# Kernel optimization log

Measured on AMD Instinct MI355X. Metric: run time of the kernel, lower is better.

## Reference

```python
import jax, jax.numpy as jnp
import numpy as np

B, S, F_IN, E = 8, 1024, 256, 512
INNER = 2 * E            # mLSTM proj_factor = 2.0
NH = 4                   # mLSTM num_heads
DH = INNER // NH
KS = 4                   # causal conv1d kernel size
QKV_BS = 4               # qkv_proj_blocksize
NB = INNER // QKV_BS     # number of block-diagonal qkv blocks


def setup_inputs() -> dict:
    key = jax.random.key(0)
    ks = jax.random.split(key, 16)
    g = lambda k, shape, scale: jax.random.normal(k, shape, jnp.float32) * scale
    return {
        "x": g(ks[0], (B, S, F_IN), 1.0),
        "W_in": g(ks[1], (E, F_IN), F_IN ** -0.5),
        "b_in": jnp.zeros((E,), jnp.float32),
        "ln1_w": jnp.ones((E,), jnp.float32),
        "W_up": g(ks[2], (2 * INNER, E), E ** -0.5),
        "conv_w": g(ks[3], (INNER, 1, KS), KS ** -0.5),
        "conv_b": jnp.zeros((INNER,), jnp.float32),
        "Wq": g(ks[4], (NB, QKV_BS, QKV_BS), QKV_BS ** -0.5),
        "Wk": g(ks[5], (NB, QKV_BS, QKV_BS), QKV_BS ** -0.5),
        "Wv": g(ks[6], (NB, QKV_BS, QKV_BS), QKV_BS ** -0.5),
        "W_ig": g(ks[7], (NH, 3 * INNER), (3 * INNER) ** -0.5),
        "b_ig": jnp.zeros((NH,), jnp.float32),
        "W_fg": g(ks[8], (NH, 3 * INNER), (3 * INNER) ** -0.5),
        "b_fg": jnp.linspace(3.0, 6.0, NH, dtype=jnp.float32),  # xlstm fgate bias init
        "mhln_w": jnp.ones((INNER,), jnp.float32),
        "skip": jnp.ones((INNER,), jnp.float32),
        "W_down": g(ks[9], (E, INNER), INNER ** -0.5),
        "ln_post_w": jnp.ones((E,), jnp.float32),
    }


def _ln(h, w, eps=1e-5):
    m = h.mean(-1, keepdims=True)
    v = jnp.mean((h - m) ** 2, axis=-1, keepdims=True)
    return (h - m) * jax.lax.rsqrt(v + eps) * w


def _causal_conv(x, w, b):
    # x: (B,S,C) -> depthwise causal conv, kernel KS, left-pad KS-1
    y = jax.lax.conv_general_dilated(
        x.transpose(0, 2, 1), w, (1,), [(KS - 1, 0)],
        dimension_numbers=("NCH", "OIH", "NCH"), feature_group_count=INNER)
    return y.transpose(0, 2, 1) + b


def _headwise(x, W):
    # block-diagonal linear (LinearHeadwiseExpand, bias=False)
    b, s, _ = x.shape
    xh = x.reshape(b, s, NB, QKV_BS)
    return jnp.einsum("bsni,noi->bsno", xh, W).reshape(b, s, -1)


def reference(x, W_in, b_in, ln1_w, W_up, conv_w, conv_b, Wq, Wk, Wv,
              W_ig, b_ig, W_fg, b_fg, mhln_w, skip, W_down, ln_post_w):
    # input proj (+ dropout = identity in eval)
    xp = x @ W_in.T + b_in                                  # (B,S,E)
    res = xp
    h = _ln(xp, ln1_w)                                      # pre-LN of mLSTM block
    up = h @ W_up.T                                         # (B,S,2*INNER)
    x_m, z = up[..., :INNER], up[..., INNER:]
    xc = jax.nn.silu(_causal_conv(x_m, conv_w, conv_b))     # (B,S,INNER)
    q = _headwise(xc, Wq)
    k = _headwise(xc, Wk)
    v = _headwise(x_m, Wv)
    gate_in = jnp.concatenate([q, k, v], axis=-1)           # (B,S,3*INNER)
    ig = (gate_in @ W_ig.T + b_ig).transpose(0, 2, 1)       # (B,NH,S)
    fg = (gate_in @ W_fg.T + b_fg).transpose(0, 2, 1)       # (B,NH,S)
    to_h = lambda t: t.reshape(B, S, NH, DH).transpose(0, 2, 1, 3)
    qh, kh, vh = to_h(q), to_h(k), to_h(v)                  # (B,NH,S,DH)
    # --- parallel_stabilized_simple mLSTM backend ---
    logf = jax.nn.log_sigmoid(fg)                           # (B,NH,S)
    a = jnp.concatenate([jnp.zeros_like(logf[..., :1]), jnp.cumsum(logf, -1)], -1)
    M = a[..., :, None] - a[..., None, :]                   # (B,NH,S+1,S+1)
    mask = jnp.tril(jnp.ones((S + 1, S + 1), bool))
    logD = jnp.where(mask, M, -jnp.inf)[..., 1:, 1:] + ig[..., None, :]
    maxD = logD.max(-1, keepdims=True)                      # (B,NH,S,1)
    D = jnp.exp(logD - maxD)
    C = jnp.einsum("bnsd,bntd->bnst", qh, kh * (DH ** -0.5)) * D
    n = jnp.maximum(jnp.abs(C.sum(-1, keepdims=True)), jnp.exp(-maxD))
    hh = jnp.einsum("bnst,bntd->bnsd", C / (n + 1e-6), vh)  # (B,NH,S,DH)
    # multi-head layernorm (GroupNorm per head, weight only, bias-free)
    hn = hh.transpose(0, 2, 1, 3)                           # (B,S,NH,DH)
    mu = hn.mean(-1, keepdims=True)
    var = jnp.mean((hn - mu) ** 2, axis=-1, keepdims=True)
    hn = (hn - mu) * jax.lax.rsqrt(var + 1e-5) * mhln_w.reshape(NH, DH)
    hn = hn.reshape(B, S, INNER)
    h_state = (hn + skip * xc) * jax.nn.silu(z)             # learnable skip + output gate
    y = h_state @ W_down.T                                  # (B,S,E)
    out = res + y                                           # residual
    return _ln(out, ln_post_w)                              # post_blocks_norm
```

## Files before the change

### kernel.cpp

```cpp
#include <hip/hip_runtime.h>

#define S_LEN 1024
#define B_SZ 8
#define F_IN_D 256
#define E_DIM 512
#define INNER_D 1024
#define NH_D 4
#define DH_D 256
#define NROW (B_SZ * S_LEN)

typedef _Float16 half8 __attribute__((ext_vector_type(8)));
typedef _Float16 half4_t __attribute__((ext_vector_type(4)));
typedef float v4f __attribute__((ext_vector_type(4)));

__global__ __launch_bounds__(256) void cast4_kernel(
    const float* __restrict__ s0, const float* __restrict__ s1,
    const float* __restrict__ s2, const float* __restrict__ s3,
    _Float16* __restrict__ d0, _Float16* __restrict__ d1,
    _Float16* __restrict__ d2, _Float16* __restrict__ d3,
    int n0, int n1, int n2, int n3)
{
  int i = (blockIdx.x * 256 + threadIdx.x) * 4;
  const float* s; _Float16* d; int off;
  if (i < n0)                { s = s0; d = d0; off = i; }
  else if (i < n0 + n1)      { s = s1; d = d1; off = i - n0; }
  else if (i < n0 + n1 + n2) { s = s2; d = d2; off = i - n0 - n1; }
  else if (i < n0 + n1 + n2 + n3) { s = s3; d = d3; off = i - n0 - n1 - n2; }
  else return;
  float4 v = *(const float4*)(s + off);
  half4_t o = {(_Float16)v.x, (_Float16)v.y, (_Float16)v.z, (_Float16)v.w};
  *(half4_t*)(d + off) = o;
}

#define GBM 128
#define GBN 128
#define GBK 64
#define LDKG (GBK + 8)

__global__ __launch_bounds__(256) void gemm_h16(
    const _Float16* __restrict__ A, const _Float16* __restrict__ B,
    const float* __restrict__ bias, float* __restrict__ C,
    int M, int N, int K)
{
  __shared__ __align__(16) _Float16 As[GBM][LDKG];
  __shared__ __align__(16) _Float16 Bs[GBN][LDKG];
  const int tid = threadIdx.x;
  const int lane = tid & 63, w = tid >> 6;
  const int wr = w >> 1, wc = w & 1;
  const int quad = lane >> 4, l16 = lane & 15;
  const int bm = blockIdx.y * GBM, bn = blockIdx.x * GBN;
  const int srow = tid >> 1;
  const int scol = (tid & 1) * 32;

  v4f acc[4][4];
#pragma unroll
  for (int i = 0; i < 4; ++i)
#pragma unroll
    for (int j = 0; j < 4; ++j) acc[i][j] = (v4f){0.f, 0.f, 0.f, 0.f};

  const _Float16* Ap = A + (size_t)(bm + srow) * K + scol;
  const _Float16* Bp = B + (size_t)(bn + srow) * K + scol;
  half8 ap[4], bp[4];
#pragma unroll
  for (int j = 0; j < 4; ++j) {
    ap[j] = *(const half8*)(Ap + j * 8);
    bp[j] = *(const half8*)(Bp + j * 8);
  }

  for (int k0 = 0; k0 < K; k0 += GBK) {
    __syncthreads();
#pragma unroll
    for (int j = 0; j < 4; ++j) {
      *(half8*)(&As[srow][scol + j * 8]) = ap[j];
      *(half8*)(&Bs[srow][scol + j * 8]) = bp[j];
    }
    __syncthreads();
    if (k0 + GBK < K) {
      const int kn = k0 + GBK;
#pragma unroll
      for (int j = 0; j < 4; ++j) {
        ap[j] = *(const half8*)(Ap + kn + j * 8);
        bp[j] = *(const half8*)(Bp + kn + j * 8);
      }
    }
#pragma unroll
    for (int kc = 0; kc < 2; ++kc) {
      half8 af[4], bf[4];
#pragma unroll
      for (int i = 0; i < 4; ++i)
        af[i] = *(const half8*)(&As[wr * 64 + i * 16 + l16][kc * 32 + quad * 8]);
#pragma unroll
      for (int j = 0; j < 4; ++j)
        bf[j] = *(const half8*)(&Bs[wc * 64 + j * 16 + l16][kc * 32 + quad * 8]);
#pragma unroll
      for (int i = 0; i < 4; ++i)
#pragma unroll
        for (int j = 0; j < 4; ++j)
          acc[i][j] = __builtin_amdgcn_mfma_f32_16x16x32_f16(af[i], bf[j], acc[i][j], 0, 0, 0);
    }
  }

#pragma unroll
  for (int j = 0; j < 4; ++j) {
    const int col = bn + wc * 64 + j * 16 + l16;
    const float bv = bias ? bias[col] : 0.f;
#pragma unroll
    for (int i = 0; i < 4; ++i) {
      const int row0 = bm + wr * 64 + i * 16 + quad * 4;
#pragma unroll
      for (int r = 0; r < 4; ++r)
        C[(size_t)(row0 + r) * N + col] = acc[i][j][r] + bv;
    }
  }
}

__global__ __launch_bounds__(256) void gemm_h16_up(
    const _Float16* __restrict__ A, const _Float16* __restrict__ B,
    _Float16* __restrict__ xmh, _Float16* __restrict__ szb,
    int M, int N, int K)
{
  __shared__ __align__(16) _Float16 As[GBM][LDKG];
  __shared__ __align__(16) _Float16 Bs[GBN][LDKG];
  const int tid = threadIdx.x;
  const int lane = tid & 63, w = tid >> 6;
  const int wr = w >> 1, wc = w & 1;
  const int quad = lane >> 4, l16 = lane & 15;
  const int bm = blockIdx.y * GBM, bn = blockIdx.x * GBN;
  const int srow = tid >> 1;
  const int scol = (tid & 1) * 32;

  v4f acc[4][4];
#pragma unroll
  for (int i = 0; i < 4; ++i)
#pragma unroll
    for (int j = 0; j < 4; ++j) acc[i][j] = (v4f){0.f, 0.f, 0.f, 0.f};

  const _Float16* Ap = A + (size_t)(bm + srow) * K + scol;
  const _Float16* Bp = B + (size_t)(bn + srow) * K + scol;
  half8 ap[4], bp[4];
#pragma unroll
  for (int j = 0; j < 4; ++j) {
    ap[j] = *(const half8*)(Ap + j * 8);
    bp[j] = *(const half8*)(Bp + j * 8);
  }

  for (int k0 = 0; k0 < K; k0 += GBK) {
    __syncthreads();
#pragma unroll
    for (int j = 0; j < 4; ++j) {
      *(half8*)(&As[srow][scol + j * 8]) = ap[j];
      *(half8*)(&Bs[srow][scol + j * 8]) = bp[j];
    }
    __syncthreads();
    if (k0 + GBK < K) {
      const int kn = k0 + GBK;
#pragma unroll
      for (int j = 0; j < 4; ++j) {
        ap[j] = *(const half8*)(Ap + kn + j * 8);
        bp[j] = *(const half8*)(Bp + kn + j * 8);
      }
    }
#pragma unroll
    for (int kc = 0; kc < 2; ++kc) {
      half8 af[4], bf[4];
#pragma unroll
      for (int i = 0; i < 4; ++i)
        af[i] = *(const half8*)(&As[wr * 64 + i * 16 + l16][kc * 32 + quad * 8]);
#pragma unroll
      for (int j = 0; j < 4; ++j)
        bf[j] = *(const half8*)(&Bs[wc * 64 + j * 16 + l16][kc * 32 + quad * 8]);
#pragma unroll
      for (int i = 0; i < 4; ++i)
#pragma unroll
        for (int j = 0; j < 4; ++j)
          acc[i][j] = __builtin_amdgcn_mfma_f32_16x16x32_f16(af[i], bf[j], acc[i][j], 0, 0, 0);
    }
  }

  const bool zhalf = (bn >= INNER_D);
#pragma unroll
  for (int j = 0; j < 4; ++j) {
    const int col = bn + wc * 64 + j * 16 + l16;
    const int colm = col & (INNER_D - 1);
#pragma unroll
    for (int i = 0; i < 4; ++i) {
      const int row0 = bm + wr * 64 + i * 16 + quad * 4;
#pragma unroll
      for (int r = 0; r < 4; ++r) {
        float a = acc[i][j][r];
        if (zhalf) {
          float s = a / (1.f + __expf(-a));
          szb[(size_t)(row0 + r) * INNER_D + colm] = (_Float16)s;
        } else {
          xmh[(size_t)(row0 + r) * INNER_D + colm] = (_Float16)a;
        }
      }
    }
  }
}

__device__ __forceinline__ float block_sum4(float v, float* red, int tid) {
#pragma unroll
  for (int off = 32; off; off >>= 1) v += __shfl_xor(v, off);
  if ((tid & 63) == 0) red[tid >> 6] = v;
  __syncthreads();
  float t = red[0] + red[1] + red[2] + red[3];
  __syncthreads();
  return t;
}

__global__ __launch_bounds__(256) void ln_mul_kernel(
    const float* __restrict__ in, const float* __restrict__ w,
    _Float16* __restrict__ out)
{
  __shared__ float red[4];
  const int row = blockIdx.x;
  const int tid = threadIdx.x;
  const float* p = in + (size_t)row * E_DIM;
  float v0 = p[tid], v1 = p[tid + 256];
  float mean = block_sum4(v0 + v1, red, tid) * (1.f / E_DIM);
  float d0 = v0 - mean, d1 = v1 - mean;
  float var = block_sum4(d0 * d0 + d1 * d1, red, tid) * (1.f / E_DIM);
  float rstd = rsqrtf(var + 1e-5f);
  out[(size_t)row * E_DIM + tid] = (_Float16)(d0 * rstd * w[tid]);
  out[(size_t)row * E_DIM + tid + 256] = (_Float16)(d1 * rstd * w[tid + 256]);
}

__global__ __launch_bounds__(256) void final_ln_kernel(
    const float* __restrict__ res, const float* __restrict__ y,
    const float* __restrict__ w, float* __restrict__ out)
{
  __shared__ float red[4];
  const int row = blockIdx.x;
  const int tid = threadIdx.x;
  const size_t base = (size_t)row * E_DIM;
  float v0 = res[base + tid] + y[base + tid];
  float v1 = res[base + tid + 256] + y[base + tid + 256];
  float mean = block_sum4(v0 + v1, red, tid) * (1.f / E_DIM);
  float d0 = v0 - mean, d1 = v1 - mean;
  float var = block_sum4(d0 * d0 + d1 * d1, red, tid) * (1.f / E_DIM);
  float rstd = rsqrtf(var + 1e-5f);
  out[base + tid] = d0 * rstd * w[tid];
  out[base + tid + 256] = d1 * rstd * w[tid + 256];
}

__global__ __launch_bounds__(256) void chg_kernel(
    const _Float16* __restrict__ xm, const float* __restrict__ cw,
    const float* __restrict__ cb,
    const float* __restrict__ Wq, const float* __restrict__ Wk,
    const float* __restrict__ Wv,
    const float* __restrict__ Wig, const float* __restrict__ big,
    const float* __restrict__ Wfg, const float* __restrict__ bfg,
    _Float16* __restrict__ xch, _Float16* __restrict__ qh,
    _Float16* __restrict__ khb, _Float16* __restrict__ vhb,
    float* __restrict__ ig, float* __restrict__ fg)
{
  __shared__ float red[4][32];
  const int tid = threadIdx.x;
  const int lane = tid & 63, wid = tid >> 6;
  const int row0 = blockIdx.x * 4;
  const int sl0 = row0 & (S_LEN - 1);
  const int c = tid * 4;

  float t[7][4];
#pragma unroll
  for (int j = 0; j < 7; ++j) {
    const int off = j - 3;
    if (sl0 + off < 0) {
      t[j][0] = t[j][1] = t[j][2] = t[j][3] = 0.f;
    } else {
      half4_t hv = *(const half4_t*)(xm + (size_t)(row0 + off) * INNER_D + c);
      t[j][0] = (float)hv.x; t[j][1] = (float)hv.y;
      t[j][2] = (float)hv.z; t[j][3] = (float)hv.w;
    }
  }
  float wct[4][4];
#pragma unroll
  for (int j = 0; j < 4; ++j) {
    float4 wc4 = *(const float4*)(cw + (c + j) * 4);
    wct[j][0] = wc4.x; wct[j][1] = wc4.y; wct[j][2] = wc4.z; wct[j][3] = wc4.w;
  }
  float4 cb4 = *(const float4*)(cb + c);
  const float cbs[4] = {cb4.x, cb4.y, cb4.z, cb4.w};
  float wqm[16], wkm[16], wvm[16];
#pragma unroll
  for (int i = 0; i < 4; ++i) {
    float4 a = *(const float4*)(Wq + tid * 16 + i * 4);
    float4 bq = *(const float4*)(Wk + tid * 16 + i * 4);
    float4 cq = *(const float4*)(Wv + tid * 16 + i * 4);
    wqm[i * 4] = a.x; wqm[i * 4 + 1] = a.y; wqm[i * 4 + 2] = a.z; wqm[i * 4 + 3] = a.w;
    wkm[i * 4] = bq.x; wkm[i * 4 + 1] = bq.y; wkm[i * 4 + 2] = bq.z; wkm[i * 4 + 3] = bq.w;
    wvm[i * 4] = cq.x; wvm[i * 4 + 1] = cq.y; wvm[i * 4 + 2] = cq.z; wvm[i * 4 + 3] = cq.w;
  }

  float q4[4][4], k4[4][4], v4m[4][4];
#pragma unroll
  for (int r = 0; r < 4; ++r) {
    float xc4[4];
#pragma unroll
    for (int j = 0; j < 4; ++j) {
      float a = cbs[j] + wct[j][0] * t[r][j] + wct[j][1] * t[r + 1][j]
                       + wct[j][2] * t[r + 2][j] + wct[j][3] * t[r + 3][j];
      xc4[j] = a / (1.f + __expf(-a));
    }
#pragma unroll
    for (int i = 0; i < 4; ++i) {
      q4[r][i] = wqm[i * 4] * xc4[0] + wqm[i * 4 + 1] * xc4[1]
               + wqm[i * 4 + 2] * xc4[2] + wqm[i * 4 + 3] * xc4[3];
      k4[r][i] = wkm[i * 4] * xc4[0] + wkm[i * 4 + 1] * xc4[1]
               + wkm[i * 4 + 2] * xc4[2] + wkm[i * 4 + 3] * xc4[3];
      v4m[r][i] = wvm[i * 4] * t[r + 3][0] + wvm[i * 4 + 1] * t[r + 3][1]
                + wvm[i * 4 + 2] * t[r + 3][2] + wvm[i * 4 + 3] * t[r + 3][3];
    }
    const size_t base = (size_t)(row0 + r) * INNER_D + c;
    half4_t xo = {(_Float16)xc4[0], (_Float16)xc4[1], (_Float16)xc4[2], (_Float16)xc4[3]};
    half4_t qo = {(_Float16)q4[r][0], (_Float16)q4[r][1], (_Float16)q4[r][2], (_Float16)q4[r][3]};
    half4_t ko = {(_Float16)k4[r][0], (_Float16)k4[r][1], (_Float16)k4[r][2], (_Float16)k4[r][3]};
    half4_t vo = {(_Float16)v4m[r][0], (_Float16)v4m[r][1], (_Float16)v4m[r][2], (_Float16)v4m[r][3]};
    *(half4_t*)(xch + base) = xo;
    *(half4_t*)(qh + base) = qo;
    *(half4_t*)(khb + base) = ko;
    *(half4_t*)(vhb + base) = vo;
  }

  float vals[32];
#pragma unroll
  for (int g = 0; g < 8; ++g) {
    const float* wb = (g < 4 ? Wig : Wfg) + (g & 3) * 3072 + c;
    float4 w1 = *(const float4*)(wb);
    float4 w2 = *(const float4*)(wb + 1024);
    float4 w3 = *(const float4*)(wb + 2048);
#pragma unroll
    for (int r = 0; r < 4; ++r) {
      vals[g * 4 + r] =
          q4[r][0] * w1.x + q4[r][1] * w1.y + q4[r][2] * w1.z + q4[r][3] * w1.w
        + k4[r][0] * w2.x + k4[r][1] * w2.y + k4[r][2] * w2.z + k4[r][3] * w2.w
        + v4m[r][0] * w3.x + v4m[r][1] * w3.y + v4m[r][2] * w3.z + v4m[r][3] * w3.w;
    }
  }
#pragma unroll
  for (int i = 0; i < 32; ++i) {
    float x = vals[i];
#pragma unroll
    for (int off = 32; off; off >>= 1) x += __shfl_xor(x, off);
    vals[i] = x;
  }
  if (lane == 0) {
#pragma unroll
    for (int i = 0; i < 32; ++i) red[wid][i] = vals[i];
  }
  __syncthreads();
  if (tid < 32) {
    float sm = red[0][tid] + red[1][tid] + red[2][tid] + red[3][tid];
    const int g = tid >> 2, r = tid & 3;
    const int h = g & 3;
    const int b = row0 >> 10;
    const size_t oidx = (size_t)(b * NH_D + h) * S_LEN + sl0 + r;
    if (g < 4) ig[oidx] = sm + big[h];
    else       fg[oidx] = sm + bfg[h];
  }
}

__device__ __forceinline__ float logsigf(float x) {
  return fminf(x, 0.f) - log1pf(__expf(-fabsf(x)));
}

__global__ __launch_bounds__(256) void scan_kernel(
    const float* __restrict__ ig, const float* __restrict__ fg,
    float* __restrict__ m_, float* __restrict__ rmax_, float* __restrict__ maxd_,
    float* __restrict__ em_)
{
  __shared__ float sc[256];
  const int bh = blockIdx.x;
  const int tid = threadIdx.x;
  const size_t base = (size_t)bh * S_LEN + tid * 4;
  float4 f4 = *(const float4*)(fg + base);
  float4 i4 = *(const float4*)(ig + base);
  float l0 = logsigf(f4.x), l1 = logsigf(f4.y), l2 = logsigf(f4.z), l3 = logsigf(f4.w);
  float p0 = l0, p1 = p0 + l1, p2 = p1 + l2, p3 = p2 + l3;
  sc[tid] = p3;
  __syncthreads();
  for (int off = 1; off < 256; off <<= 1) {
    float o = (tid >= off) ? sc[tid - off] : 0.f;
    __syncthreads();
    sc[tid] += o;
    __syncthreads();
  }
  float aoff = (tid == 0) ? 0.f : sc[tid - 1];
  __syncthreads();
  float a0 = aoff + p0, a1 = aoff + p1, a2 = aoff + p2, a3 = aoff + p3;
  float m0 = i4.x - a0, m1 = i4.y - a1, m2 = i4.z - a2, m3 = i4.w - a3;
  float x0 = m0, x1 = fmaxf(x0, m1), x2 = fmaxf(x1, m2), x3 = fmaxf(x2, m3);
  sc[tid] = x3;
  __syncthreads();
  for (int off = 1; off < 256; off <<= 1) {
    float o = (tid >= off) ? sc[tid - off] : -1e30f;
    __syncthreads();
    sc[tid] = fmaxf(sc[tid], o);
    __syncthreads();
  }
  float moff = (tid == 0) ? -1e30f : sc[tid - 1];
  float tmax = sc[tid | 15];
  float r0 = fmaxf(moff, x0), r1 = fmaxf(moff, x1), r2 = fmaxf(moff, x2), r3 = fmaxf(moff, x3);
  const float scale = 0.0625f;
  float4 mo = {m0, m1, m2, m3};
  float4 ro = {r0, r1, r2, r3};
  float4 dd = {a0 + r0, a1 + r1, a2 + r2, a3 + r3};
  float4 eo = {scale * __expf(m0 - tmax), scale * __expf(m1 - tmax),
               scale * __expf(m2 - tmax), scale * __expf(m3 - tmax)};
  *(float4*)(m_ + base) = mo;
  *(float4*)(rmax_ + base) = ro;
  *(float4*)(maxd_ + base) = dd;
  *(float4*)(em_ + base) = eo;
}

__global__ __launch_bounds__(256) void vtrans_kernel(
    const _Float16* __restrict__ vb, _Float16* __restrict__ vt)
{
  __shared__ _Float16 tile[64][68];
  const int b = blockIdx.z, dt = blockIdx.x, st = blockIdx.y;
  const int c4 = (threadIdx.x & 15) * 4, rr = threadIdx.x >> 4;
  const int s0 = st * 64, d0 = dt * 64;
#pragma unroll
  for (int i = 0; i < 4; ++i) {
    int r = rr + i * 16;
    half4_t v = *(const half4_t*)(vb + ((size_t)(b * S_LEN + s0 + r)) * INNER_D + d0 + c4);
    tile[r][c4 + 0] = v.x; tile[r][c4 + 1] = v.y;
    tile[r][c4 + 2] = v.z; tile[r][c4 + 3] = v.w;
  }
  __syncthreads();
#pragma unroll
  for (int i = 0; i < 4; ++i) {
    int dd = rr + i * 16;
    half4_t o = {tile[c4 + 0][dd], tile[c4 + 1][dd], tile[c4 + 2][dd], tile[c4 + 3][dd]};
    *(half4_t*)(vt + ((size_t)(b * INNER_D + d0 + dd)) * S_LEN + s0 + c4) = o;
  }
}

#define KP 264
#define VP 72
#define PP 72

__global__ __launch_bounds__(256, 2) void attn_blk_kernel(
    const _Float16* __restrict__ qh, const _Float16* __restrict__ khb,
    const _Float16* __restrict__ vt,
    const float* __restrict__ m_, const float* __restrict__ em,
    const float* __restrict__ rmax_, const float* __restrict__ maxd_,
    const float* __restrict__ mhln_w, const float* __restrict__ skip,
    const _Float16* __restrict__ xch, const _Float16* __restrict__ szb,
    _Float16* __restrict__ hstate)
{
  __shared__ __align__(16) _Float16 Ks[64][KP];
  __shared__ __align__(16) _Float16 Vs[256][VP];
  __shared__ __align__(16) _Float16 Pl[64][PP];
  __shared__ float cred[2][64];
  const int tid = threadIdx.x;
  const int lane = tid & 63, wid = tid >> 6;
  const int quad = lane >> 4, l16 = lane & 15;
  const int wr = wid >> 1;
  const int ws = wid & 1;
  const int bh = blockIdx.x & 31;
  int pp = blockIdx.x >> 5;
  if (pp >= 8) pp = 23 - pp;
  const int sblk = 15 - pp;
  const int h = bh & 3, b = bh >> 2;
  const float* rmaxp = rmax_ + (size_t)bh * S_LEN;
  const float* emp = em + (size_t)bh * S_LEN;
  const float* mp = m_ + (size_t)bh * S_LEN;
  const float* maxdp = maxd_ + (size_t)bh * S_LEN;
  const float scale = 0.0625f;

  const _Float16* kg = khb + ((size_t)(b * S_LEN)) * INNER_D + h * DH_D;
  const _Float16* vg = vt + ((size_t)(b * INNER_D + h * DH_D)) * S_LEN;
  const int krow_s = tid >> 5;
  const int kcol_s = (tid & 31) * 8;
  const int vrow_s = tid >> 3;
  const int vcol_s = (tid & 7) * 8;

  const int ntile = sblk + 1;
  const int qb0 = sblk * 64;

  half8 kpre[8], vpre[8];
#pragma unroll
  for (int i = 0; i < 8; ++i) {
    kpre[i] = *(const half8*)(kg + (size_t)(i * 8 + krow_s) * INNER_D + kcol_s);
    vpre[i] = *(const half8*)(vg + (size_t)(i * 32 + vrow_s) * S_LEN + vcol_s);
  }

  half8 qf[2][8];
#pragma unroll
  for (int g = 0; g < 2; ++g) {
    const _Float16* qrow =
        qh + ((size_t)(b * S_LEN + qb0 + wr * 32 + g * 16 + l16)) * INNER_D
           + h * DH_D + quad * 8;
#pragma unroll
    for (int c = 0; c < 8; ++c) qf[g][c] = *(const half8*)(qrow + c * 32);
  }

  v4f acc[2][8];
#pragma unroll
  for (int g = 0; g < 2; ++g)
#pragma unroll
    for (int nc = 0; nc < 8; ++nc) acc[g][nc] = (v4f){0.f, 0.f, 0.f, 0.f};
  float rsum[8] = {0.f, 0.f, 0.f, 0.f, 0.f, 0.f, 0.f, 0.f};
  float rmax_row[8];
#pragma unroll
  for (int g = 0; g < 2; ++g)
#pragma unroll
    for (int r = 0; r < 4; ++r)
      rmax_row[g * 4 + r] = rmaxp[qb0 + wr * 32 + g * 16 + quad * 4 + r];

  for (int tt = 0; tt < ntile; ++tt) {
    const int t0 = tt * 64;
    const bool last = (tt + 1 == ntile);
    __syncthreads();
#pragma unroll
    for (int i = 0; i < 8; ++i) {
      *(half8*)(&Ks[i * 8 + krow_s][kcol_s]) = kpre[i];
      *(half8*)(&Vs[i * 32 + vrow_s][vcol_s]) = vpre[i];
    }
    __syncthreads();
    if (!last) {
      const int tn = t0 + 64;
#pragma unroll
      for (int i = 0; i < 8; ++i) {
        kpre[i] = *(const half8*)(kg + (size_t)(tn + i * 8 + krow_s) * INNER_D + kcol_s);
        vpre[i] = *(const half8*)(vg + (size_t)(i * 32 + vrow_s) * S_LEN + tn + vcol_s);
      }
    }
    float rowfac[8];
    if (!last) {
      const float rtile = rmaxp[t0 + 63];
#pragma unroll
      for (int gr = 0; gr < 8; ++gr) rowfac[gr] = __expf(rtile - rmax_row[gr]);
    }
#pragma unroll
    for (int ks = 0; ks < 2; ++ks) {
      v4f sg[2];
      sg[0] = (v4f){0.f, 0.f, 0.f, 0.f};
      sg[1] = (v4f){0.f, 0.f, 0.f, 0.f};
#pragma unroll
      for (int c = 0; c < 8; ++c) {
        half8 kf = *(const half8*)(&Ks[ws * 32 + ks * 16 + l16][c * 32 + quad * 8]);
        sg[0] = __builtin_amdgcn_mfma_f32_16x16x32_f16(qf[0][c], kf, sg[0], 0, 0, 0);
        sg[1] = __builtin_amdgcn_mfma_f32_16x16x32_f16(qf[1][c], kf, sg[1], 0, 0, 0);
      }
      const int t = t0 + ws * 32 + ks * 16 + l16;
      if (last) {
        const float mt = mp[t];
#pragma unroll
        for (int g = 0; g < 2; ++g)
#pragma unroll
          for (int r = 0; r < 4; ++r) {
            const int srow = qb0 + wr * 32 + g * 16 + quad * 4 + r;
            float cc = (t <= srow)
                         ? sg[g][r] * scale * __expf(mt - rmax_row[g * 4 + r]) : 0.f;
            rsum[g * 4 + r] += cc;
            Pl[wr * 32 + g * 16 + quad * 4 + r][ws * 32 + ks * 16 + l16] = (_Float16)cc;
          }
      } else {
        const float emv = emp[t];
#pragma unroll
        for (int g = 0; g < 2; ++g)
#pragma unroll
          for (int r = 0; r < 4; ++r) {
            float cc = sg[g][r] * emv * rowfac[g * 4 + r];
            rsum[g * 4 + r] += cc;
            Pl[wr * 32 + g * 16 + quad * 4 + r][ws * 32 + ks * 16 + l16] = (_Float16)cc;
          }
      }
    }
    __syncthreads();
    half8 pf[2][2];
#pragma unroll
    for (int g = 0; g < 2; ++g) {
      pf[g][0] = *(const half8*)(&Pl[wr * 32 + g * 16 + l16][quad * 8]);
      pf[g][1] = *(const half8*)(&Pl[wr * 32 + g * 16 + l16][32 + quad * 8]);
    }
#pragma unroll
    for (int nc = 0; nc < 8; ++nc) {
      half8 vf0 = *(const half8*)(&Vs[ws * 128 + nc * 16 + l16][quad * 8]);
      half8 vf1 = *(const half8*)(&Vs[ws * 128 + nc * 16 + l16][32 + quad * 8]);
      acc[0][nc] = __builtin_amdgcn_mfma_f32_16x16x32_f16(pf[0][0], vf0, acc[0][nc], 0, 0, 0);
      acc[0][nc] = __builtin_amdgcn_mfma_f32_16x16x32_f16(pf[0][1], vf1, acc[0][nc], 0, 0, 0);
      acc[1][nc] = __builtin_amdgcn_mfma_f32_16x16x32_f16(pf[1][0], vf0, acc[1][nc], 0, 0, 0);
      acc[1][nc] = __builtin_amdgcn_mfma_f32_16x16x32_f16(pf[1][1], vf1, acc[1][nc], 0, 0, 0);
    }
  }

#pragma unroll
  for (int gr = 0; gr < 8; ++gr) {
    float rs = rsum[gr];
    rs += __shfl_xor(rs, 1); rs += __shfl_xor(rs, 2);
    rs += __shfl_xor(rs, 4); rs += __shfl_xor(rs, 8);
    rsum[gr] = rs;
  }
  if (l16 == 0) {
#pragma unroll
    for (int g = 0; g < 2; ++g)
#pragma unroll
      for (int r = 0; r < 4; ++r)
        cred[ws][wr * 32 + g * 16 + quad * 4 + r] = rsum[g * 4 + r];
  }
  __syncthreads();
  float inv[8];
#pragma unroll
  for (int g = 0; g < 2; ++g)
#pragma unroll
    for (int r = 0; r < 4; ++r) {
      const int row = wr * 32 + g * 16 + quad * 4 + r;
      float rs = cred[0][row] + cred[1][row];
      float md = maxdp[qb0 + row];
      float n = fmaxf(fabsf(rs), __expf(-md));
      inv[g * 4 + r] = 1.f / (n + 1e-6f);
    }
#pragma unroll
  for (int g = 0; g < 2; ++g)
#pragma unroll
    for (int nc = 0; nc < 8; ++nc)
#pragma unroll
      for (int r = 0; r < 4; ++r) acc[g][nc][r] *= inv[g * 4 + r];

  __syncthreads();
  float mean[8];
#pragma unroll
  for (int gr = 0; gr < 8; ++gr) {
    const int g = gr >> 2, r = gr & 3;
    float sm = 0.f;
#pragma unroll
    for (int nc = 0; nc < 8; ++nc) sm += acc[g][nc][r];
    sm += __shfl_xor(sm, 1); sm += __shfl_xor(sm, 2);
    sm += __shfl_xor(sm, 4); sm += __shfl_xor(sm, 8);
    if (l16 == 0) cred[ws][wr * 32 + g * 16 + quad * 4 + r] = sm;
  }
  __syncthreads();
#pragma unroll
  for (int gr = 0; gr < 8; ++gr) {
    const int g = gr >> 2, r = gr & 3;
    const int row = wr * 32 + g * 16 + quad * 4 + r;
    mean[gr] = (cred[0][row] + cred[1][row]) * (1.f / DH_D);
  }
  __syncthreads();
  float rstd[8];
#pragma unroll
  for (int gr = 0; gr < 8; ++gr) {
    const int g = gr >> 2, r = gr & 3;
    float sq = 0.f;
#pragma unroll
    for (int nc = 0; nc < 8; ++nc) { float d = acc[g][nc][r] - mean[gr]; sq += d * d; }
    sq += __shfl_xor(sq, 1); sq += __shfl_xor(sq, 2);
    sq += __shfl_xor(sq, 4); sq += __shfl_xor(sq, 8);
    if (l16 == 0) cred[ws][wr * 32 + g * 16 + quad * 4 + r] = sq;
  }
  __syncthreads();
#pragma unroll
  for (int gr = 0; gr < 8; ++gr) {
    const int g = gr >> 2, r = gr & 3;
    const int row = wr * 32 + g * 16 + quad * 4 + r;
    rstd[gr] = rsqrtf((cred[0][row] + cred[1][row]) * (1.f / DH_D) + 1e-5f);
  }

#pragma unroll
  for (int nc = 0; nc < 8; ++nc) {
    const int d = h * DH_D + ws * 128 + nc * 16 + l16;
    const float w = mhln_w[d];
    const float sk = skip[d];
#pragma unroll
    for (int g = 0; g < 2; ++g)
#pragma unroll
      for (int r = 0; r < 4; ++r) {
        const size_t row = (size_t)(b * S_LEN + qb0 + wr * 32 + g * 16 + quad * 4 + r);
        float xcv = (float)xch[row * INNER_D + d];
        float sz = (float)szb[row * INNER_D + d];
        float o = ((acc[g][nc][r] - mean[g * 4 + r]) * rstd[g * 4 + r] * w + sk * xcv) * sz;
        hstate[row * INNER_D + d] = (_Float16)o;
      }
  }
}

extern "C" void kernel_launch(void* const* d_in, const int* in_sizes, int n_in,
                              void* d_out, int out_size, void* d_ws, size_t ws_size,
                              hipStream_t stream)
{
  const float* x      = (const float*)d_in[0];
  const float* W_in   = (const float*)d_in[1];
  const float* b_in   = (const float*)d_in[2];
  const float* ln1_w  = (const float*)d_in[3];
  const float* W_up   = (const float*)d_in[4];
  const float* conv_w = (const float*)d_in[5];
  const float* conv_b = (const float*)d_in[6];
  const float* Wq     = (const float*)d_in[7];
  const float* Wk     = (const float*)d_in[8];
  const float* Wv     = (const float*)d_in[9];
  const float* W_ig   = (const float*)d_in[10];
  const float* b_ig   = (const float*)d_in[11];
  const float* W_fg   = (const float*)d_in[12];
  const float* b_fg   = (const float*)d_in[13];
  const float* mhln_w = (const float*)d_in[14];
  const float* skip   = (const float*)d_in[15];
  const float* W_down = (const float*)d_in[16];
  const float* ln_post_w = (const float*)d_in[17];
  float* out = (float*)d_out;

  float* ws = (float*)d_ws;
  size_t o = 0;
  float* xp     = ws + o; o += (size_t)NROW * E_DIM;
  float* hbuf   = ws + o; o += (size_t)NROW * E_DIM;
  _Float16* h16 = (_Float16*)(ws + o);
  size_t ho = 0;
  _Float16* xh      = h16 + ho; ho += (size_t)NROW * F_IN_D;
  _Float16* WinH    = h16 + ho; ho += (size_t)E_DIM * F_IN_D;
  _Float16* WupH    = h16 + ho; ho += (size_t)2 * INNER_D * E_DIM;
  _Float16* WdownH  = h16 + ho; ho += (size_t)E_DIM * INNER_D;
  _Float16* hh      = h16 + ho; ho += (size_t)NROW * E_DIM;
  _Float16* xmh     = h16 + ho; ho += (size_t)NROW * INNER_D;
  _Float16* szb     = h16 + ho; ho += (size_t)NROW * INNER_D;
  _Float16* xch     = h16 + ho; ho += (size_t)NROW * INNER_D;
  _Float16* qh      = h16 + ho; ho += (size_t)NROW * INNER_D;
  _Float16* khb     = h16 + ho; ho += (size_t)NROW * INNER_D;
  _Float16* vhb     = h16 + ho; ho += (size_t)NROW * INNER_D;
  _Float16* vtb     = h16 + ho; ho += (size_t)NROW * INNER_D;
  _Float16* hstateH = h16 + ho; ho += (size_t)NROW * INNER_D;

  const int GSZ = B_SZ * NH_D * S_LEN;
  float* igb   = hbuf;
  float* fgb   = hbuf + GSZ;
  float* mb    = hbuf + 2 * GSZ;
  float* rmaxb = hbuf + 3 * GSZ;
  float* maxdb = hbuf + 4 * GSZ;
  float* emb   = hbuf + 5 * GSZ;
  float* yb    = hbuf;

  dim3 blk(256);
  const int nx = NROW * F_IN_D, nwi = E_DIM * F_IN_D,
            nwu = 2 * INNER_D * E_DIM, nwd = E_DIM * INNER_D;
  const int ntot = nx + nwi + nwu + nwd;
  cast4_kernel<<<(ntot / 4 + 255) / 256, blk, 0, stream>>>(
      x, W_in, W_up, W_down, xh, WinH, WupH, WdownH, nx, nwi, nwu, nwd);
  gemm_h16<<<dim3(E_DIM / GBN, NROW / GBM), blk, 0, stream>>>(
      xh, WinH, b_in, xp, NROW, E_DIM, F_IN_D);
  ln_mul_kernel<<<NROW, blk, 0, stream>>>(xp, ln1_w, hh);
  gemm_h16_up<<<dim3(2 * INNER_D / GBN, NROW / GBM), blk, 0, stream>>>(
      hh, WupH, xmh, szb, NROW, 2 * INNER_D, E_DIM);
  chg_kernel<<<NROW / 4, blk, 0, stream>>>(
      xmh, conv_w, conv_b, Wq, Wk, Wv, W_ig, b_ig, W_fg, b_fg,
      xch, qh, khb, vhb, igb, fgb);
  scan_kernel<<<B_SZ * NH_D, blk, 0, stream>>>(igb, fgb, mb, rmaxb, maxdb, emb);
  vtrans_kernel<<<dim3(16, 16, 8), blk, 0, stream>>>(vhb, vtb);
  attn_blk_kernel<<<512, blk, 0, stream>>>(
      qh, khb, vtb, mb, emb, rmaxb, maxdb, mhln_w, skip, xch, szb, hstateH);
  gemm_h16<<<dim3(E_DIM / GBN, NROW / GBM), blk, 0, stream>>>(
      hstateH, WdownH, nullptr, yb, NROW, E_DIM, INNER_D);
  final_ln_kernel<<<NROW, blk, 0, stream>>>(xp, yb, ln_post_w, out);
}
```

Measured before the change: 283.9 us.

## Pair complementary query blocks in one 512-thread attention workgroup sharing K/V tiles

Each attention workgroup now holds two 4-wave groups that process complementary causal query blocks (j and 15-j) of the same batch-head. Both groups share each K/V tile staged in LDS, so K/V global loads and LDS staging are amortised over two query blocks. Every block also gets a balanced total of causal work. In exchange, the short-block group sits idle at barriers for the tiles beyond its causal range, the block size doubles with one block per CU, and the grid halves to 256 blocks, which can lower latency hiding.

```diff
diff --git a/kernel.cpp b/kernel.cpp
--- a/kernel.cpp
+++ b/kernel.cpp
@@ -441,7 +441,7 @@
 #define VP 72
 #define PP 72
 
-__global__ __launch_bounds__(256, 2) void attn_blk_kernel(
+__global__ __launch_bounds__(512, 1) void attn_blk_kernel(
     const _Float16* __restrict__ qh, const _Float16* __restrict__ khb,
     const _Float16* __restrict__ vt,
     const float* __restrict__ m_, const float* __restrict__ em,
@@ -452,17 +452,20 @@
 {
   __shared__ __align__(16) _Float16 Ks[64][KP];
   __shared__ __align__(16) _Float16 Vs[256][VP];
-  __shared__ __align__(16) _Float16 Pl[64][PP];
-  __shared__ float cred[2][64];
+  __shared__ __align__(16) _Float16 Pl[2][64][PP];
+  __shared__ float cred[2][2][64];
   const int tid = threadIdx.x;
   const int lane = tid & 63, wid = tid >> 6;
   const int quad = lane >> 4, l16 = lane & 15;
-  const int wr = wid >> 1;
+  const int grp = wid >> 2;
+  const int wr = (wid >> 1) & 1;
   const int ws = wid & 1;
-  const int bh = blockIdx.x & 31;
-  int pp = blockIdx.x >> 5;
-  if (pp >= 8) pp = 23 - pp;
-  const int sblk = 15 - pp;
+  const int bh = blockIdx.x >> 3;
+  const int j = blockIdx.x & 7;
+  const int qblk = grp ? j : (15 - j);
+  const int ntile = qblk + 1;
+  const int Tmax = 16 - j;
+  const int qb0 = qblk * 64;
   const int h = bh & 3, b = bh >> 2;
   const float* rmaxp = rmax_ + (size_t)bh * S_LEN;
   const float* emp = em + (size_t)bh * S_LEN;
@@ -477,14 +480,11 @@
   const int vrow_s = tid >> 3;
   const int vcol_s = (tid & 7) * 8;
 
-  const int ntile = sblk + 1;
-  const int qb0 = sblk * 64;
-
-  half8 kpre[8], vpre[8];
-#pragma unroll
-  for (int i = 0; i < 8; ++i) {
-    kpre[i] = *(const half8*)(kg + (size_t)(i * 8 + krow_s) * INNER_D + kcol_s);
-    vpre[i] = *(const half8*)(vg + (size_t)(i * 32 + vrow_s) * S_LEN + vcol_s);
+  half8 kpre[4], vpre[4];
+#pragma unroll
+  for (int i = 0; i < 4; ++i) {
+    kpre[i] = *(const half8*)(kg + (size_t)(i * 16 + krow_s) * INNER_D + kcol_s);
+    vpre[i] = *(const half8*)(vg + (size_t)(i * 64 + vrow_s) * S_LEN + vcol_s);
   }
 
   half8 qf[2][8];
@@ -510,81 +510,86 @@
     for (int r = 0; r < 4; ++r)
       rmax_row[g * 4 + r] = rmaxp[qb0 + wr * 32 + g * 16 + quad * 4 + r];
 
-  for (int tt = 0; tt < ntile; ++tt) {
+  for (int tt = 0; tt < Tmax; ++tt) {
     const int t0 = tt * 64;
-    const bool last = (tt + 1 == ntile);
-    __syncthreads();
-#pragma unroll
-    for (int i = 0; i < 8; ++i) {
-      *(half8*)(&Ks[i * 8 + krow_s][kcol_s]) = kpre[i];
-      *(half8*)(&Vs[i * 32 + vrow_s][vcol_s]) = vpre[i];
-    }
-    __syncthreads();
-    if (!last) {
+    const bool active = (tt < ntile);
+    const bool diag = (tt == ntile - 1);
+    __syncthreads();
+#pragma unroll
+    for (int i = 0; i < 4; ++i) {
+      *(half8*)(&Ks[i * 16 + krow_s][kcol_s]) = kpre[i];
+      *(half8*)(&Vs[i * 64 + vrow_s][vcol_s]) = vpre[i];
+    }
+    __syncthreads();
+    if (tt + 1 < Tmax) {
       const int tn = t0 + 64;
 #pragma unroll
-      for (int i = 0; i < 8; ++i) {
-        kpre[i] = *(const half8*)(kg + (size_t)(tn + i * 8 + krow_s) * INNER_D + kcol_s);
-        vpre[i] = *(const half8*)(vg + (size_t)(i * 32 + vrow_s) * S_LEN + tn + vcol_s);
-      }
-    }
-    float rowfac[8];
-    if (!last) {
-      const float rtile = rmaxp[t0 + 63];
-#pragma unroll
-      for (int gr = 0; gr < 8; ++gr) rowfac[gr] = __expf(rtile - rmax_row[gr]);
-    }
-#pragma unroll
-    for (int ks = 0; ks < 2; ++ks) {
-      v4f sg[2];
-      sg[0] = (v4f){0.f, 0.f, 0.f, 0.f};
-      sg[1] = (v4f){0.f, 0.f, 0.f, 0.f};
-#pragma unroll
-      for (int c = 0; c < 8; ++c) {
-        half8 kf = *(const half8*)(&Ks[ws * 32 + ks * 16 + l16][c * 32 + quad * 8]);
-        sg[0] = __builtin_amdgcn_mfma_f32_16x16x32_f16(qf[0][c], kf, sg[0], 0, 0, 0);
-        sg[1] = __builtin_amdgcn_mfma_f32_16x16x32_f16(qf[1][c], kf, sg[1], 0, 0, 0);
-      }
-      const int t = t0 + ws * 32 + ks * 16 + l16;
-      if (last) {
-        const float mt = mp[t];
-#pragma unroll
-        for (int g = 0; g < 2; ++g)
-#pragma unroll
-          for (int r = 0; r < 4; ++r) {
-            const int srow = qb0 + wr * 32 + g * 16 + quad * 4 + r;
-            float cc = (t <= srow)
-                         ? sg[g][r] * scale * __expf(mt - rmax_row[g * 4 + r]) : 0.f;
-            rsum[g * 4 + r] += cc;
-            Pl[wr * 32 + g * 16 + quad * 4 + r][ws * 32 + ks * 16 + l16] = (_Float16)cc;
-          }
-      } else {
-        const float emv = emp[t];
-#pragma unroll
-        for (int g = 0; g < 2; ++g)
-#pragma unroll
-          for (int r = 0; r < 4; ++r) {
-            float cc = sg[g][r] * emv * rowfac[g * 4 + r];
-            rsum[g * 4 + r] += cc;
-            Pl[wr * 32 + g * 16 + quad * 4 + r][ws * 32 + ks * 16 + l16] = (_Float16)cc;
-          }
-      }
-    }
-    __syncthreads();
-    half8 pf[2][2];
-#pragma unroll
-    for (int g = 0; g < 2; ++g) {
-      pf[g][0] = *(const half8*)(&Pl[wr * 32 + g * 16 + l16][quad * 8]);
-      pf[g][1] = *(const half8*)(&Pl[wr * 32 + g * 16 + l16][32 + quad * 8]);
-    }
-#pragma unroll
-    for (int nc = 0; nc < 8; ++nc) {
-      half8 vf0 = *(const half8*)(&Vs[ws * 128 + nc * 16 + l16][quad * 8]);
-      half8 vf1 = *(const half8*)(&Vs[ws * 128 + nc * 16 + l16][32 + quad * 8]);
-      acc[0][nc] = __builtin_amdgcn_mfma_f32_16x16x32_f16(pf[0][0], vf0, acc[0][nc], 0, 0, 0);
-      acc[0][nc] = __builtin_amdgcn_mfma_f32_16x16x32_f16(pf[0][1], vf1, acc[0][nc], 0, 0, 0);
-      acc[1][nc] = __builtin_amdgcn_mfma_f32_16x16x32_f16(pf[1][0], vf0, acc[1][nc], 0, 0, 0);
-      acc[1][nc] = __builtin_amdgcn_mfma_f32_16x16x32_f16(pf[1][1], vf1, acc[1][nc], 0, 0, 0);
+      for (int i = 0; i < 4; ++i) {
+        kpre[i] = *(const half8*)(kg + (size_t)(tn + i * 16 + krow_s) * INNER_D + kcol_s);
+        vpre[i] = *(const half8*)(vg + (size_t)(i * 64 + vrow_s) * S_LEN + tn + vcol_s);
+      }
+    }
+    if (active) {
+      float rowfac[8];
+      if (!diag) {
+        const float rtile = rmaxp[t0 + 63];
+#pragma unroll
+        for (int gr = 0; gr < 8; ++gr) rowfac[gr] = __expf(rtile - rmax_row[gr]);
+      }
+#pragma unroll
+      for (int ks = 0; ks < 2; ++ks) {
+        v4f sg[2];
+        sg[0] = (v4f){0.f, 0.f, 0.f, 0.f};
+        sg[1] = (v4f){0.f, 0.f, 0.f, 0.f};
+#pragma unroll
+        for (int c = 0; c < 8; ++c) {
+          half8 kf = *(const half8*)(&Ks[ws * 32 + ks * 16 + l16][c * 32 + quad * 8]);
+          sg[0] = __builtin_amdgcn_mfma_f32_16x16x32_f16(qf[0][c], kf, sg[0], 0, 0, 0);
+          sg[1] = __builtin_amdgcn_mfma_f32_16x16x32_f16(qf[1][c], kf, sg[1], 0, 0, 0);
+        }
+        const int t = t0 + ws * 32 + ks * 16 + l16;
+        if (diag) {
+          const float mt = mp[t];
+#pragma unroll
+          for (int g = 0; g < 2; ++g)
+#pragma unroll
+            for (int r = 0; r < 4; ++r) {
+              const int srow = qb0 + wr * 32 + g * 16 + quad * 4 + r;
+              float cc = (t <= srow)
+                           ? sg[g][r] * scale * __expf(mt - rmax_row[g * 4 + r]) : 0.f;
+              rsum[g * 4 + r] += cc;
+              Pl[grp][wr * 32 + g * 16 + quad * 4 + r][ws * 32 + ks * 16 + l16] = (_Float16)cc;
+            }
+        } else {
+          const float emv = emp[t];
+#pragma unroll
+          for (int g = 0; g < 2; ++g)
+#pragma unroll
+            for (int r = 0; r < 4; ++r) {
+              float cc = sg[g][r] * emv * rowfac[g * 4 + r];
+              rsum[g * 4 + r] += cc;
+              Pl[grp][wr * 32 + g * 16 + quad * 4 + r][ws * 32 + ks * 16 + l16] = (_Float16)cc;
+            }
+        }
+      }
+    }
+    __syncthreads();
+    if (active) {
+      half8 pf[2][2];
+#pragma unroll
+      for (int g = 0; g < 2; ++g) {
+        pf[g][0] = *(const half8*)(&Pl[grp][wr * 32 + g * 16 + l16][quad * 8]);
+        pf[g][1] = *(const half8*)(&Pl[grp][wr * 32 + g * 16 + l16][32 + quad * 8]);
+      }
+#pragma unroll
+      for (int nc = 0; nc < 8; ++nc) {
+        half8 vf0 = *(const half8*)(&Vs[ws * 128 + nc * 16 + l16][quad * 8]);
+        half8 vf1 = *(const half8*)(&Vs[ws * 128 + nc * 16 + l16][32 + quad * 8]);
+        acc[0][nc] = __builtin_amdgcn_mfma_f32_16x16x32_f16(pf[0][0], vf0, acc[0][nc], 0, 0, 0);
+        acc[0][nc] = __builtin_amdgcn_mfma_f32_16x16x32_f16(pf[0][1], vf1, acc[0][nc], 0, 0, 0);
+        acc[1][nc] = __builtin_amdgcn_mfma_f32_16x16x32_f16(pf[1][0], vf0, acc[1][nc], 0, 0, 0);
+        acc[1][nc] = __builtin_amdgcn_mfma_f32_16x16x32_f16(pf[1][1], vf1, acc[1][nc], 0, 0, 0);
+      }
     }
   }
 
@@ -600,7 +605,7 @@
     for (int g = 0; g < 2; ++g)
 #pragma unroll
       for (int r = 0; r < 4; ++r)
-        cred[ws][wr * 32 + g * 16 + quad * 4 + r] = rsum[g * 4 + r];
+        cred[grp][ws][wr * 32 + g * 16 + quad * 4 + r] = rsum[g * 4 + r];
   }
   __syncthreads();
   float inv[8];
@@ -609,7 +614,7 @@
 #pragma unroll
     for (int r = 0; r < 4; ++r) {
       const int row = wr * 32 + g * 16 + quad * 4 + r;
-      float rs = cred[0][row] + cred[1][row];
+      float rs = cred[grp][0][row] + cred[grp][1][row];
       float md = maxdp[qb0 + row];
       float n = fmaxf(fabsf(rs), __expf(-md));
       inv[g * 4 + r] = 1.f / (n + 1e-6f);
@@ -631,14 +636,14 @@
     for (int nc = 0; nc < 8; ++nc) sm += acc[g][nc][r];
     sm += __shfl_xor(sm, 1); sm += __shfl_xor(sm, 2);
     sm += __shfl_xor(sm, 4); sm += __shfl_xor(sm, 8);
-    if (l16 == 0) cred[ws][wr * 32 + g * 16 + quad * 4 + r] = sm;
+    if (l16 == 0) cred[grp][ws][wr * 32 + g * 16 + quad * 4 + r] = sm;
   }
   __syncthreads();
 #pragma unroll
   for (int gr = 0; gr < 8; ++gr) {
     const int g = gr >> 2, r = gr & 3;
     const int row = wr * 32 + g * 16 + quad * 4 + r;
-    mean[gr] = (cred[0][row] + cred[1][row]) * (1.f / DH_D);
+    mean[gr] = (cred[grp][0][row] + cred[grp][1][row]) * (1.f / DH_D);
   }
   __syncthreads();
   float rstd[8];
@@ -650,14 +655,14 @@
     for (int nc = 0; nc < 8; ++nc) { float d = acc[g][nc][r] - mean[gr]; sq += d * d; }
     sq += __shfl_xor(sq, 1); sq += __shfl_xor(sq, 2);
     sq += __shfl_xor(sq, 4); sq += __shfl_xor(sq, 8);
-    if (l16 == 0) cred[ws][wr * 32 + g * 16 + quad * 4 + r] = sq;
+    if (l16 == 0) cred[grp][ws][wr * 32 + g * 16 + quad * 4 + r] = sq;
   }
   __syncthreads();
 #pragma unroll
   for (int gr = 0; gr < 8; ++gr) {
     const int g = gr >> 2, r = gr & 3;
     const int row = wr * 32 + g * 16 + quad * 4 + r;
-    rstd[gr] = rsqrtf((cred[0][row] + cred[1][row]) * (1.f / DH_D) + 1e-5f);
+    rstd[gr] = rsqrtf((cred[grp][0][row] + cred[grp][1][row]) * (1.f / DH_D) + 1e-5f);
   }
 
 #pragma unroll
@@ -747,7 +752,7 @@
       xch, qh, khb, vhb, igb, fgb);
   scan_kernel<<<B_SZ * NH_D, blk, 0, stream>>>(igb, fgb, mb, rmaxb, maxdb, emb);
   vtrans_kernel<<<dim3(16, 16, 8), blk, 0, stream>>>(vhb, vtb);
-  attn_blk_kernel<<<512, blk, 0, stream>>>(
+  attn_blk_kernel<<<256, dim3(512), 0, stream>>>(
       qh, khb, vtb, mb, emb, rmaxb, maxdb, mhln_w, skip, xch, szb, hstateH);
   gemm_h16<<<dim3(E_DIM / GBN, NROW / GBM), blk, 0, stream>>>(
       hstateH, WdownH, nullptr, yb, NROW, E_DIM, INNER_D);
```

New measurement: 285.1 us. No clear change (+0.4%).
